# Kernel optimization log

Hardware: AMD Instinct MI355X
Metric: run time of the kernel (lower is better)

## Reference

```python
import jax, jax.numpy as jnp
import numpy as np

EMBEDDING_DIM = 256
NUM_EMBEDDINGS = 8192
COMMITMENT_COST = 0.25
DECAY = 0.99
EPSILON = 1e-5


def setup_inputs() -> dict:
    key = jax.random.key(0)
    k1, k2 = jax.random.split(key)
    inputs = jax.random.normal(k1, (16, 32, 32, EMBEDDING_DIM), dtype=jnp.float32)
    # VarianceScaling(distribution='uniform'), fan_in scaling over [D, K]
    limit = float(np.sqrt(3.0 / EMBEDDING_DIM))
    embeddings = jax.random.uniform(k2, (EMBEDDING_DIM, NUM_EMBEDDINGS),
                                    minval=-limit, maxval=limit, dtype=jnp.float32)
    return {
        'inputs': inputs,
        'embeddings': embeddings,
        'ema_cs_hidden': jnp.zeros((NUM_EMBEDDINGS,), jnp.float32),
        'ema_dw_hidden': embeddings,  # hk initializes ema_dw to the embeddings
        'counter': 0,
        'is_training': 1,
    }


def reference(inputs, embeddings, ema_cs_hidden, ema_dw_hidden, counter, is_training):
    flat = inputs.reshape(-1, EMBEDDING_DIM)                        # [N, D]
    distances = (jnp.sum(flat ** 2, axis=1, keepdims=True)
                 - 2.0 * (flat @ embeddings)
                 + jnp.sum(embeddings ** 2, axis=0, keepdims=True))  # [N, K]
    encoding_indices = jnp.argmax(-distances, axis=1)                # [N]
    encodings = jax.nn.one_hot(encoding_indices, NUM_EMBEDDINGS,
                               dtype=distances.dtype)                # [N, K]
    idx = encoding_indices.reshape(inputs.shape[:-1])
    quantized = embeddings.T[idx]                                    # gather codebook
    e_latent_loss = jnp.mean((jax.lax.stop_gradient(quantized) - inputs) ** 2)
    loss = COMMITMENT_COST * e_latent_loss

    if is_training:
        # haiku ExponentialMovingAverage with zero-debias
        new_counter = counter + 1
        debias = 1.0 - DECAY ** new_counter
        cs_hidden = ema_cs_hidden * DECAY + jnp.sum(encodings, axis=0) * (1.0 - DECAY)
        cs_avg = cs_hidden / debias                                  # [K]
        dw = flat.T @ encodings                                      # [D, K] scatter-add as GEMM
        dw_hidden = ema_dw_hidden * DECAY + dw * (1.0 - DECAY)
        dw_avg = dw_hidden / debias
        n = jnp.sum(cs_avg)
        cs_norm = (cs_avg + EPSILON) / (n + NUM_EMBEDDINGS * EPSILON) * n
        new_embeddings = dw_avg / cs_norm[None, :]                   # [D, K]
    else:
        new_embeddings = embeddings

    # straight-through estimator
    quantized_st = inputs + jax.lax.stop_gradient(quantized - inputs)
    avg_probs = jnp.mean(encodings, axis=0)
    perplexity = jnp.exp(-jnp.sum(avg_probs * jnp.log(avg_probs + 1e-10)))
    return (quantized_st, loss, perplexity, idx, new_embeddings)
```

## Files before the change

### kernel.cpp

```cpp
#include <hip/hip_runtime.h>
#include <math.h>

#define DD 256
#define KK 8192
#define NN 16384
#define DECAYF 0.99f
#define EPSF 1e-5f
#define TAU 4e-3f

#define O_Q    0
#define O_LOSS 4194304
#define O_PERP 4194305
#define O_IDX  4194306
#define O_EMB  4210690

typedef float f32x4 __attribute__((ext_vector_type(4)));
typedef _Float16 f16x8 __attribute__((ext_vector_type(8)));

__device__ __forceinline__ unsigned short f2h(float f) {
  union { _Float16 h; unsigned short u; } c;
  c.h = (_Float16)f;
  return c.u;
}

__device__ __forceinline__ void gll16(const void* g, void* l) {
  __builtin_amdgcn_global_load_lds((const __attribute__((address_space(1))) void*)g,
                                   (__attribute__((address_space(3))) void*)l, 16, 0, 0);
}

#define DPPI(x, ctrl) __builtin_amdgcn_update_dpp((x), (x), (ctrl), 0xf, 0xf, true)
#define DPPF(x, ctrl) __int_as_float(__builtin_amdgcn_update_dpp(__float_as_int(x), __float_as_int(x), (ctrl), 0xf, 0xf, true))

__global__ void k_convert_xe(const float* __restrict__ x, unsigned short* __restrict__ Ah,
                             const float* __restrict__ emb, unsigned short* __restrict__ Eh,
                             float* __restrict__ embT, float* __restrict__ esqp,
                             unsigned long long* __restrict__ keysR,
                             float* __restrict__ counts, float* __restrict__ loss_part,
                             int* __restrict__ listc) {
  __shared__ float ld[32 * 33];
  int bx = blockIdx.x;
  int t = threadIdx.x;
  if (bx < 4096) {
    int i = bx * 256 + t;
    float4 v = ((const float4*)x)[i];
    ushort4 h;
    h.x = f2h(v.x); h.y = f2h(v.y); h.z = f2h(v.z); h.w = f2h(v.w);
    ((ushort4*)Ah)[i] = h;
    if (bx < 64) {
      keysR[bx * 256 + t] = ~0ull;
    } else if (bx < 96) {
      counts[(bx - 64) * 256 + t] = 0.f;
    } else if (bx == 96) {
      loss_part[t] = 0.f;
      if (t == 0) *listc = 0;
    }
    return;
  }
  int eb = bx - 4096;
  int k0 = (eb & 255) * 32, d0b = eb >> 8;
  {
    int din = t >> 3, kq = (t & 7) * 4;
    float4 v = *(const float4*)(emb + (size_t)(d0b * 32 + din) * KK + k0 + kq);
    ld[din * 33 + kq + 0] = v.x; ld[din * 33 + kq + 1] = v.y;
    ld[din * 33 + kq + 2] = v.z; ld[din * 33 + kq + 3] = v.w;
  }
  __syncthreads();
  int kout = t >> 3, dq = (t & 7) * 4;
  float f0 = ld[(dq + 0) * 33 + kout], f1 = ld[(dq + 1) * 33 + kout];
  float f2 = ld[(dq + 2) * 33 + kout], f3 = ld[(dq + 3) * 33 + kout];
  size_t o = (size_t)(k0 + kout) * DD + d0b * 32 + dq;
  float4 fv; fv.x = f0; fv.y = f1; fv.z = f2; fv.w = f3;
  *(float4*)(embT + o) = fv;
  ushort4 hv;
  hv.x = f2h(f0); hv.y = f2h(f1); hv.z = f2h(f2); hv.w = f2h(f3);
  *(ushort4*)(Eh + o) = hv;
  float p = (f0 * f0 + f1 * f1) + (f2 * f2 + f3 * f3);
  p += __shfl_xor(p, 1, 64);
  p += __shfl_xor(p, 2, 64);
  p += __shfl_xor(p, 4, 64);
  if ((t & 7) == 0) esqp[(size_t)(k0 + kout) * 8 + d0b] = p;
}

__launch_bounds__(256, 2)
__global__ void k_dist_mfma(const unsigned short* __restrict__ Ah, const unsigned short* __restrict__ Bh,
                            const float* __restrict__ esqp,
                            float* __restrict__ part1, float* __restrict__ part2,
                            int* __restrict__ partidx) {
  __shared__ __align__(16) unsigned short sB[8192];
  __shared__ float sEq[128];

  const int tid = threadIdx.x;
  const int w = tid >> 6, lane = tid & 63;
  const int kb = blockIdx.x, nb = blockIdx.y;
  const int row0 = nb * 128, col0 = kb * 128;
  const int m = lane & 15, q = lane >> 4;

  size_t gB[4];
  int lbB[4];
  #pragma unroll
  for (int s = 0; s < 4; ++s) {
    int g = w * 4 + s;
    int r = g * 8 + (lane >> 3);
    int c = (lane & 7) ^ (r & 7);
    gB[s] = (size_t)(col0 + r) * DD + c * 8;
    lbB[s] = g * 512;
  }

  const unsigned short* pA0 = Ah + (size_t)(row0 + w * 32 + m) * DD + q * 8;
  const unsigned short* pA1 = pA0 + 16 * DD;

  f32x4 acc[2][8];
  #pragma unroll
  for (int i = 0; i < 2; ++i)
    #pragma unroll
    for (int j = 0; j < 8; ++j) acc[i][j] = (f32x4)0.f;

  for (int it = 0; it < 4; ++it) {
    const int d0 = it * 64;
    __syncthreads();
    #pragma unroll
    for (int s = 0; s < 4; ++s) gll16(Bh + gB[s] + d0, sB + lbB[s]);
    f16x8 a[2][2];
    #pragma unroll
    for (int kk = 0; kk < 2; ++kk) {
      a[kk][0] = *(const f16x8*)(pA0 + d0 + kk * 32);
      a[kk][1] = *(const f16x8*)(pA1 + d0 + kk * 32);
    }
    __syncthreads();
    #pragma unroll
    for (int kk = 0; kk < 2; ++kk) {
      #pragma unroll
      for (int j = 0; j < 8; ++j) {
        int cn = j * 16 + m;
        int slot = (kk * 4 + q) ^ (cn & 7);
        f16x8 b = *(const f16x8*)(sB + cn * 64 + slot * 8);
        acc[0][j] = __builtin_amdgcn_mfma_f32_16x16x32_f16(a[kk][0], b, acc[0][j], 0, 0, 0);
        acc[1][j] = __builtin_amdgcn_mfma_f32_16x16x32_f16(a[kk][1], b, acc[1][j], 0, 0, 0);
      }
    }
  }

  {
    int col = tid >> 1, half = tid & 1;
    const float4* ep = (const float4*)esqp + (size_t)(col0 + col) * 2 + half;
    float4 s = *ep;
    float p = (s.x + s.y) + (s.z + s.w);
    p += __shfl_xor(p, 1, 64);
    if (half == 0) sEq[col] = p;
  }
  __syncthreads();

  float eq[8];
  #pragma unroll
  for (int j = 0; j < 8; ++j) eq[j] = sEq[j * 16 + m];

  #define RSTAGE(CTRL) {                                  \
    float ov = DPPF(m1, CTRL);                            \
    int   oi = DPPI(bi, CTRL);                            \
    float o2 = DPPF(m2, CTRL);                            \
    m2 = fminf(fminf(m2, o2), fmaxf(m1, ov));             \
    bool p = ov < m1;                                     \
    m1 = fminf(m1, ov);                                   \
    bi = p ? oi : bi;                                     \
  }
  #pragma unroll
  for (int i = 0; i < 2; ++i) {
    #pragma unroll
    for (int reg = 0; reg < 4; ++reg) {
      float m1 = 3.402823466e+38f, m2 = 3.402823466e+38f;
      int bi = 0;
      #pragma unroll
      for (int j = 0; j < 8; ++j) {
        float dd = fmaf(-2.0f, acc[i][j][reg], eq[j]);
        bool p = dd < m1;
        m2 = fminf(m2, fmaxf(dd, m1));
        m1 = fminf(m1, dd);
        bi = p ? (col0 + j * 16 + m) : bi;
      }
      RSTAGE(0xB1)
      RSTAGE(0x4E)
      RSTAGE(0x141)
      RSTAGE(0x140)
      if (m == 0) {
        int prow = row0 + w * 32 + i * 16 + q * 4 + reg;
        int pidx = kb * NN + prow;
        part1[pidx] = m1; part2[pidx] = m2; partidx[pidx] = bi;
      }
    }
  }
  #undef RSTAGE
}

__global__ void k_argmin2(float* __restrict__ part1, float* __restrict__ part2,
                          const int* __restrict__ partidx, int* __restrict__ idxw,
                          int* __restrict__ listc, int* __restrict__ list) {
  int row = blockIdx.x * 256 + threadIdx.x;
  float m1 = 3.402823466e+38f, m2 = 3.402823466e+38f;
  int bi = 0;
  for (int kb = 0; kb < 64; ++kb) {
    int f = kb * NN + row;
    float a1 = part1[f], a2 = part2[f];
    int ai = partidx[f];
    part1[f] = 0.f;
    part2[f] = 0.f;
    m2 = fminf(fminf(m2, a2), fmaxf(m1, a1));
    bool p = a1 < m1;
    m1 = fminf(m1, a1);
    bi = p ? ai : bi;
  }
  idxw[row] = bi;
  if (m2 - m1 < TAU) { int pos = atomicAdd(listc, 1); list[pos] = row; }
}

__global__ void k_rescore(const float* __restrict__ x, const float* __restrict__ emb,
                          const int* __restrict__ listc, const int* __restrict__ list,
                          unsigned long long* __restrict__ keysR) {
  __shared__ float se[8192];
  __shared__ double red[256];
  const int t = threadIdx.x;
  const int k0 = blockIdx.x * 32;
  int cnt = *listc;
  if ((int)blockIdx.y >= cnt) return;
  #pragma unroll
  for (int i = 0; i < 32; ++i) {
    int elem = i * 256 + t;
    int d = elem >> 5, c = elem & 31;
    se[d * 32 + c] = emb[(size_t)d * KK + k0 + c];
  }
  __syncthreads();
  const int c = t & 31, p = t >> 5;
  for (int li = blockIdx.y; li < cnt; li += gridDim.y) {
    int row = list[li];
    const float* xr = x + (size_t)row * DD;
    double acc = 0.0;
    #pragma unroll
    for (int j = 0; j < 32; ++j) {
      int d = p * 32 + j;
      double df = (double)xr[d] - (double)se[d * 32 + c];
      acc = fma(df, df, acc);
    }
    red[c * 8 + p] = acc;
    __syncthreads();
    if (t < 64) {
      unsigned long long key = ~0ull;
      if (t < 32) {
        double dist = 0.0;
        #pragma unroll
        for (int qq = 0; qq < 8; ++qq) dist += red[t * 8 + qq];
        key = ((unsigned long long)__double_as_longlong(dist) & ~0x1FFFull)
              | (unsigned long long)(k0 + t);
      }
      #pragma unroll
      for (int s = 1; s < 64; s <<= 1) {
        unsigned long long o = __shfl_xor(key, s, 64);
        if (o < key) key = o;
      }
      if (t == 0) atomicMin(&keysR[row], key);
    }
    __syncthreads();
  }
}

__global__ void k_gather(const float* __restrict__ x, const float* __restrict__ embT,
                         const int* __restrict__ idxw, const unsigned long long* __restrict__ keysR,
                         const int* __restrict__ train,
                         float* __restrict__ outq, float* __restrict__ outidx,
                         float* __restrict__ dwT, float* __restrict__ counts,
                         float* __restrict__ loss_part) {
  int w = threadIdx.x >> 6, l = threadIdx.x & 63;
  int n = blockIdx.x * 4 + w;
  unsigned long long kv = keysR[n];
  int k = (kv != ~0ull) ? (int)(kv & 0x1FFFull) : idxw[n];
  float4 xv = ((const float4*)(x + (size_t)n * DD))[l];
  float4 qv = ((const float4*)(embT + (size_t)k * DD))[l];
  int d = l * 4;

  ((float4*)(outq + (size_t)n * DD))[l] = qv;

  float e0 = qv.x - xv.x, e1 = qv.y - xv.y, e2 = qv.z - xv.z, e3 = qv.w - xv.w;
  float ls = (e0 * e0 + e1 * e1) + (e2 * e2 + e3 * e3);

  if (*train) {
    const float wdw = 1.0f - DECAYF;
    float* base = dwT + (size_t)k * DD + d;
    atomicAdd(base + 0, xv.x * wdw);
    atomicAdd(base + 1, xv.y * wdw);
    atomicAdd(base + 2, xv.z * wdw);
    atomicAdd(base + 3, xv.w * wdw);
  }

  #pragma unroll
  for (int s = 1; s < 64; s <<= 1) ls += __shfl_xor(ls, s, 64);
  if (l == 0) {
    atomicAdd(&loss_part[blockIdx.x & 255], ls);
    atomicAdd(&counts[k], 1.0f);
    outidx[n] = (float)k;
  }
}

__global__ void k_final(const float* __restrict__ dwT, const float* __restrict__ ema_dw,
                        const float* __restrict__ emb, const float* __restrict__ counts,
                        const float* __restrict__ ema_cs, const float* __restrict__ loss_part,
                        const int* __restrict__ counter, const int* __restrict__ train,
                        float* __restrict__ out4, float* __restrict__ outloss,
                        float* __restrict__ outperp) {
  __shared__ float ld[32 * 33];
  __shared__ float s_red[4], s_l[4], s_e[4];
  __shared__ float csn_s[32];
  int t = threadIdx.x;
  int k0 = blockIdx.x * 32, d0 = blockIdx.y * 32;
  int w = t >> 6, lane = t & 63;

  if (blockIdx.x == 0 && blockIdx.y == 0) {
    float lloc = loss_part[t];
    float eloc = 0.f;
    for (int i = 0; i < 32; ++i) {
      float cc = counts[t + i * 256];
      float pp = cc * (1.0f / 16384.0f);
      eloc += pp * logf(pp + 1e-10f);
    }
    #pragma unroll
    for (int s = 1; s < 64; s <<= 1) {
      lloc += __shfl_xor(lloc, s, 64);
      eloc += __shfl_xor(eloc, s, 64);
    }
    if (lane == 0) { s_l[w] = lloc; s_e[w] = eloc; }
    __syncthreads();
    if (t == 0) {
      outloss[0] = 0.25f * (((s_l[0] + s_l[1]) + (s_l[2] + s_l[3])) / 4194304.0f);
      outperp[0] = expf(-((s_e[0] + s_e[1]) + (s_e[2] + s_e[3])));
    }
  }

  if (*train) {
    float debias = 1.0f - powf(DECAYF, (float)(*counter + 1));
    float inv = 1.0f / debias;
    float nloc = 0.f;
    for (int i = 0; i < 32; ++i) {
      int k = t + i * 256;
      nloc += fmaf(counts[k], 1.0f - DECAYF, ema_cs[k] * DECAYF);
    }
    #pragma unroll
    for (int s = 1; s < 64; s <<= 1) nloc += __shfl_xor(nloc, s, 64);
    if (lane == 0) s_red[w] = nloc;
    __syncthreads();
    float nsum = ((s_red[0] + s_red[1]) + (s_red[2] + s_red[3])) * inv;
    if (t < 32) {
      int k = k0 + t;
      float a = fmaf(counts[k], 1.0f - DECAYF, ema_cs[k] * DECAYF) * inv;
      csn_s[t] = (a + EPSF) / (nsum + 8192.0f * EPSF) * nsum;
    }
    {
      int ki = t >> 3, dq = (t & 7) * 4;
      float4 v = *(const float4*)(dwT + (size_t)(k0 + ki) * DD + d0 + dq);
      ld[ki * 33 + dq + 0] = v.x; ld[ki * 33 + dq + 1] = v.y;
      ld[ki * 33 + dq + 2] = v.z; ld[ki * 33 + dq + 3] = v.w;
    }
    __syncthreads();
    int dout = t >> 3, kq = (t & 7) * 4;
    size_t o = (size_t)(d0 + dout) * KK + k0 + kq;
    float4 e = *(const float4*)(ema_dw + o);
    float4 r;
    r.x = fmaf(e.x, DECAYF, ld[(kq + 0) * 33 + dout]) * inv / csn_s[kq + 0];
    r.y = fmaf(e.y, DECAYF, ld[(kq + 1) * 33 + dout]) * inv / csn_s[kq + 1];
    r.z = fmaf(e.z, DECAYF, ld[(kq + 2) * 33 + dout]) * inv / csn_s[kq + 2];
    r.w = fmaf(e.w, DECAYF, ld[(kq + 3) * 33 + dout]) * inv / csn_s[kq + 3];
    *(float4*)(out4 + o) = r;
  } else {
    int dout = t >> 3, kq = (t & 7) * 4;
    size_t o = (size_t)(d0 + dout) * KK + k0 + kq;
    *(float4*)(out4 + o) = *(const float4*)(emb + o);
  }
}

extern "C" void kernel_launch(void* const* d_in, const int* in_sizes, int n_in,
                              void* d_out, int out_size, void* d_ws, size_t ws_size,
                              hipStream_t stream) {
  (void)in_sizes; (void)n_in; (void)out_size; (void)ws_size;
  const float* x      = (const float*)d_in[0];
  const float* emb    = (const float*)d_in[1];
  const float* ema_cs = (const float*)d_in[2];
  const float* ema_dw = (const float*)d_in[3];
  const int*   counter = (const int*)d_in[4];
  const int*   train   = (const int*)d_in[5];

  float* out = (float*)d_out;
  float* outq    = out + O_Q;
  float* outloss = out + O_LOSS;
  float* outperp = out + O_PERP;
  float* outidx  = out + O_IDX;
  float* out4    = out + O_EMB;

  char* W = (char*)d_ws;
  unsigned short* Ah   = (unsigned short*)(W);
  unsigned short* Eh   = (unsigned short*)(W + 8388608);
  float* embT          = (float*)(W + 12582912);
  float* part1         = (float*)(W + 20971520);
  float* part2         = (float*)(W + 25165824);
  int*   partidx       = (int*)(W + 29360128);
  float* dwT           = part1;
  unsigned long long* keysR = (unsigned long long*)(W + 33554432);
  float* esqp          = (float*)(W + 33685504);
  float* counts        = (float*)(W + 33947648);
  float* loss_part     = (float*)(W + 33980416);
  int*   listc         = (int*)(W + 33981440);
  int*   list          = (int*)(W + 33981444);
  int*   idxw          = (int*)(W + 34046980);

  k_convert_xe<<<6144, 256, 0, stream>>>(x, Ah, emb, Eh, embT, esqp, keysR, counts, loss_part, listc);
  k_dist_mfma<<<dim3(64, 128), 256, 0, stream>>>(Ah, Eh, esqp, part1, part2, partidx);
  k_argmin2<<<64, 256, 0, stream>>>(part1, part2, partidx, idxw, listc, list);
  k_rescore<<<dim3(256, 8), 256, 0, stream>>>(x, emb, listc, list, keysR);
  k_gather<<<4096, 256, 0, stream>>>(x, embT, idxw, keysR, train, outq, outidx, dwT, counts, loss_part);
  k_final<<<dim3(256, 8), 256, 0, stream>>>(dwT, ema_dw, emb, counts, ema_cs, loss_part, counter, train, out4, outloss, outperp);
}
```

Before: 354.5 us.

## Use 2x2 wave tiling in distance GEMM and merge column halves in LDS

Each block's four waves now form a 2x2 grid, each covering 64 rows by 64 columns of the 128x128 tile, instead of each wave covering 32 rows by all 128 columns. This cuts LDS B-fragment reads per MFMA, since each B load now feeds four MFMAs instead of two, at the cost of more A-fragment global loads. The two column halves' partial min/second-min/index values are combined through shared memory before a single write per row. The argmin2 launch is resized to 128 blocks of 128 threads for more parallelism.

After: 407.4 us. 14.9% more time.

```diff
diff --git a/kernel.cpp b/kernel.cpp
--- a/kernel.cpp
+++ b/kernel.cpp
@@ -88,9 +88,12 @@
                             int* __restrict__ partidx) {
   __shared__ __align__(16) unsigned short sB[8192];
   __shared__ float sEq[128];
+  __shared__ float sP1[256], sP2[256];
+  __shared__ int   sPi[256];
 
   const int tid = threadIdx.x;
   const int w = tid >> 6, lane = tid & 63;
+  const int wr = w >> 1, wc = w & 1;
   const int kb = blockIdx.x, nb = blockIdx.y;
   const int row0 = nb * 128, col0 = kb * 128;
   const int m = lane & 15, q = lane >> 4;
@@ -106,36 +109,37 @@
     lbB[s] = g * 512;
   }
 
-  const unsigned short* pA0 = Ah + (size_t)(row0 + w * 32 + m) * DD + q * 8;
-  const unsigned short* pA1 = pA0 + 16 * DD;
-
-  f32x4 acc[2][8];
-  #pragma unroll
-  for (int i = 0; i < 2; ++i)
-    #pragma unroll
-    for (int j = 0; j < 8; ++j) acc[i][j] = (f32x4)0.f;
+  const unsigned short* pA = Ah + (size_t)(row0 + wr * 64 + m) * DD + q * 8;
+
+  f32x4 acc[4][4];
+  #pragma unroll
+  for (int i = 0; i < 4; ++i)
+    #pragma unroll
+    for (int j = 0; j < 4; ++j) acc[i][j] = (f32x4)0.f;
 
   for (int it = 0; it < 4; ++it) {
     const int d0 = it * 64;
     __syncthreads();
     #pragma unroll
     for (int s = 0; s < 4; ++s) gll16(Bh + gB[s] + d0, sB + lbB[s]);
-    f16x8 a[2][2];
+    f16x8 a[4];
+    #pragma unroll
+    for (int i = 0; i < 4; ++i) a[i] = *(const f16x8*)(pA + i * 16 * DD + d0);
+    __syncthreads();
     #pragma unroll
     for (int kk = 0; kk < 2; ++kk) {
-      a[kk][0] = *(const f16x8*)(pA0 + d0 + kk * 32);
-      a[kk][1] = *(const f16x8*)(pA1 + d0 + kk * 32);
-    }
-    __syncthreads();
-    #pragma unroll
-    for (int kk = 0; kk < 2; ++kk) {
+      if (kk == 1) {
+        #pragma unroll
+        for (int i = 0; i < 4; ++i) a[i] = *(const f16x8*)(pA + i * 16 * DD + d0 + 32);
+      }
       #pragma unroll
-      for (int j = 0; j < 8; ++j) {
-        int cn = j * 16 + m;
+      for (int j = 0; j < 4; ++j) {
+        int cn = wc * 64 + j * 16 + m;
         int slot = (kk * 4 + q) ^ (cn & 7);
         f16x8 b = *(const f16x8*)(sB + cn * 64 + slot * 8);
-        acc[0][j] = __builtin_amdgcn_mfma_f32_16x16x32_f16(a[kk][0], b, acc[0][j], 0, 0, 0);
-        acc[1][j] = __builtin_amdgcn_mfma_f32_16x16x32_f16(a[kk][1], b, acc[1][j], 0, 0, 0);
+        #pragma unroll
+        for (int i = 0; i < 4; ++i)
+          acc[i][j] = __builtin_amdgcn_mfma_f32_16x16x32_f16(a[i], b, acc[i][j], 0, 0, 0);
       }
     }
   }
@@ -150,9 +154,9 @@
   }
   __syncthreads();
 
-  float eq[8];
-  #pragma unroll
-  for (int j = 0; j < 8; ++j) eq[j] = sEq[j * 16 + m];
+  float eq[4];
+  #pragma unroll
+  for (int j = 0; j < 4; ++j) eq[j] = sEq[wc * 64 + j * 16 + m];
 
   #define RSTAGE(CTRL) {                                  \
     float ov = DPPF(m1, CTRL);                            \
@@ -164,37 +168,48 @@
     bi = p ? oi : bi;                                     \
   }
   #pragma unroll
-  for (int i = 0; i < 2; ++i) {
+  for (int i = 0; i < 4; ++i) {
     #pragma unroll
     for (int reg = 0; reg < 4; ++reg) {
       float m1 = 3.402823466e+38f, m2 = 3.402823466e+38f;
       int bi = 0;
       #pragma unroll
-      for (int j = 0; j < 8; ++j) {
+      for (int j = 0; j < 4; ++j) {
         float dd = fmaf(-2.0f, acc[i][j][reg], eq[j]);
         bool p = dd < m1;
         m2 = fminf(m2, fmaxf(dd, m1));
         m1 = fminf(m1, dd);
-        bi = p ? (col0 + j * 16 + m) : bi;
+        bi = p ? (col0 + wc * 64 + j * 16 + m) : bi;
       }
       RSTAGE(0xB1)
       RSTAGE(0x4E)
       RSTAGE(0x141)
       RSTAGE(0x140)
       if (m == 0) {
-        int prow = row0 + w * 32 + i * 16 + q * 4 + reg;
-        int pidx = kb * NN + prow;
-        part1[pidx] = m1; part2[pidx] = m2; partidx[pidx] = bi;
+        int r = wr * 64 + i * 16 + q * 4 + reg;
+        sP1[wc * 128 + r] = m1;
+        sP2[wc * 128 + r] = m2;
+        sPi[wc * 128 + r] = bi;
       }
     }
   }
   #undef RSTAGE
+  __syncthreads();
+  if (tid < 128) {
+    float a1 = sP1[tid],       a2 = sP2[tid];
+    float b1 = sP1[128 + tid], b2 = sP2[128 + tid];
+    float mm1 = fminf(a1, b1);
+    float mm2 = fminf(fminf(a2, b2), fmaxf(a1, b1));
+    int ii = (b1 < a1) ? sPi[128 + tid] : sPi[tid];
+    int pidx = kb * NN + row0 + tid;
+    part1[pidx] = mm1; part2[pidx] = mm2; partidx[pidx] = ii;
+  }
 }
 
 __global__ void k_argmin2(float* __restrict__ part1, float* __restrict__ part2,
                           const int* __restrict__ partidx, int* __restrict__ idxw,
                           int* __restrict__ listc, int* __restrict__ list) {
-  int row = blockIdx.x * 256 + threadIdx.x;
+  int row = blockIdx.x * 128 + threadIdx.x;
   float m1 = 3.402823466e+38f, m2 = 3.402823466e+38f;
   int bi = 0;
   for (int kb = 0; kb < 64; ++kb) {
@@ -409,7 +424,7 @@
 
   k_convert_xe<<<6144, 256, 0, stream>>>(x, Ah, emb, Eh, embT, esqp, keysR, counts, loss_part, listc);
   k_dist_mfma<<<dim3(64, 128), 256, 0, stream>>>(Ah, Eh, esqp, part1, part2, partidx);
-  k_argmin2<<<64, 256, 0, stream>>>(part1, part2, partidx, idxw, listc, list);
+  k_argmin2<<<128, 128, 0, stream>>>(part1, part2, partidx, idxw, listc, list);
   k_rescore<<<dim3(256, 8), 256, 0, stream>>>(x, emb, listc, list, keysR);
   k_gather<<<4096, 256, 0, stream>>>(x, embT, idxw, keysR, train, outq, outidx, dwT, counts, loss_part);
   k_final<<<dim3(256, 8), 256, 0, stream>>>(dwT, ema_dw, emb, counts, ema_cs, loss_part, counter, train, out4, outloss, outperp);
```
